# Performance work log

Measured on AMD Instinct MI355X. Metric: run time of the kernel, lower is better.

Reference implementation:

```python
import jax, jax.numpy as jnp
import numpy as np

K = 2  # top-k experts per token


def setup_inputs() -> dict:
    key = jax.random.key(0)
    ks = jax.random.split(key, 5)
    N, D, F, E = 8192, 1024, 1024, 8
    s = lambda d: 1.0 / np.sqrt(d)
    return {
        "x": jax.random.normal(ks[0], (N, D), jnp.float32),
        "Wr": jax.random.normal(ks[1], (D, E), jnp.float32) * s(D),
        "br": jax.random.normal(ks[2], (E,), jnp.float32) * 0.01,
        "We": jax.random.normal(ks[3], (E, D, F), jnp.float32) * s(D),
        "be": jax.random.normal(ks[4], (E, F), jnp.float32) * 0.01,
    }


def reference(x, Wr, br, We, be):
    # Router: logits [N, E] -> top-k -> softmax over the k selected logits
    logits = x @ Wr + br
    topv, idx = jax.lax.top_k(logits, K)            # [N, K]
    w = jax.nn.softmax(topv, axis=-1)               # [N, K]
    # All-expert dense compute (eval mode: dropout is identity)
    h = jnp.einsum("nd,edf->nef", x, We) + be       # [N, E, F]
    h = jax.nn.gelu(h, approximate=False)           # exact GELU (torch nn.GELU default)
    # Gather the k selected experts per token and combine
    sel = jnp.take_along_axis(h, idx[:, :, None], axis=1)  # [N, K, F]
    out = jnp.einsum("nk,nkf->nf", w, sel)          # [N, F]
    return out
```

## Files before the change

kernel.cpp:

```cpp
#include <hip/hip_runtime.h>
#include <hip/hip_bf16.h>
#include <math.h>
#include <stdint.h>

#define N_TOK 8192
#define DIM   1024
#define FDIM  1024
#define NEXP  8

typedef unsigned short u16;
typedef __bf16 bf16x8 __attribute__((ext_vector_type(8)));
typedef float  f32x4  __attribute__((ext_vector_type(4)));

__device__ __forceinline__ u16 f2bf(float f) {
  union { float f; uint32_t u; } v; v.f = f;
  return (u16)((v.u + 0x7fffu + ((v.u >> 16) & 1u)) >> 16);
}

__global__ __launch_bounds__(256) void k_prep(
    const float* __restrict__ x, const float* __restrict__ Wr,
    const float* __restrict__ br, const float* __restrict__ We,
    u16* __restrict__ xb, u16* __restrict__ WeT,
    int* __restrict__ topk_idx, float* __restrict__ topk_w0) {
  __shared__ float tile[64][65];
  int b = blockIdx.x;
  if (b < 2048) {
    int n = b * 4 + (threadIdx.x >> 6);
    int lane = threadIdx.x & 63;
    const float4* xr = (const float4*)(x + (size_t)n * DIM);
    ushort4* xbr = (ushort4*)(xb + (size_t)n * DIM);
    double acc[8];
#pragma unroll
    for (int e = 0; e < 8; ++e) acc[e] = 0.0;
#pragma unroll
    for (int i = 0; i < 4; ++i) {
      int d4 = lane + 64 * i;
      float4 v = xr[d4];
      ushort4 o;
      o.x = f2bf(v.x); o.y = f2bf(v.y); o.z = f2bf(v.z); o.w = f2bf(v.w);
      xbr[d4] = o;
      float vv[4] = {v.x, v.y, v.z, v.w};
      const float* wr = Wr + (size_t)d4 * 4 * NEXP;
#pragma unroll
      for (int j = 0; j < 4; ++j) {
        float4 w0 = *(const float4*)(wr + j * 8);
        float4 w1 = *(const float4*)(wr + j * 8 + 4);
        acc[0] += (double)vv[j] * w0.x; acc[1] += (double)vv[j] * w0.y;
        acc[2] += (double)vv[j] * w0.z; acc[3] += (double)vv[j] * w0.w;
        acc[4] += (double)vv[j] * w1.x; acc[5] += (double)vv[j] * w1.y;
        acc[6] += (double)vv[j] * w1.z; acc[7] += (double)vv[j] * w1.w;
      }
    }
#pragma unroll
    for (int e = 0; e < 8; ++e) {
      for (int off = 32; off; off >>= 1) acc[e] += __shfl_xor(acc[e], off);
    }
    if (lane == 0) {
      double lg[8];
#pragma unroll
      for (int e = 0; e < 8; ++e) lg[e] = acc[e] + (double)br[e];
      int i0 = 0; double v0 = lg[0];
#pragma unroll
      for (int e = 1; e < 8; ++e) if (lg[e] > v0) { v0 = lg[e]; i0 = e; }
      int i1 = -1; double v1 = -1e300;
#pragma unroll
      for (int e = 0; e < 8; ++e) if (e != i0 && lg[e] > v1) { v1 = lg[e]; i1 = e; }
      float w0 = 1.0f / (1.0f + expf((float)(v1 - v0)));
      topk_idx[n] = i0 | (i1 << 8);
      topk_w0[n] = w0;
    }
  } else {
    int tb = b - 2048;
    int e = tb >> 8;
    int d0 = ((tb >> 4) & 15) * 64, f0 = (tb & 15) * 64;
    int t = threadIdx.x;
    int lr = t >> 6, lc = t & 63;
    const float* src = We + (size_t)e * DIM * FDIM + (size_t)d0 * FDIM + f0;
#pragma unroll
    for (int i = 0; i < 16; ++i)
      tile[i * 4 + lr][lc] = src[(size_t)(i * 4 + lr) * FDIM + lc];
    __syncthreads();
    u16* dst = WeT + (size_t)e * FDIM * DIM + (size_t)f0 * DIM + d0;
#pragma unroll
    for (int i = 0; i < 16; ++i)
      dst[(size_t)(i * 4 + lr) * DIM + lc] = f2bf(tile[lc][i * 4 + lr]);
  }
}

__global__ __launch_bounds__(256) void k_build_lists(const int* __restrict__ topk_idx,
                                                     int* __restrict__ gcount,
                                                     int* __restrict__ token_list) {
  __shared__ int lcount[8];
  __shared__ int lbase[8];
  int t = threadIdx.x;
  int n = blockIdx.x * 256 + t;
  if (t < 8) lcount[t] = 0;
  __syncthreads();
  int pk = topk_idx[n];
  int e0 = pk & 0xff, e1 = (pk >> 8) & 0xff;
  int p0 = atomicAdd(&lcount[e0], 1);
  int p1 = atomicAdd(&lcount[e1], 1);
  __syncthreads();
  if (t < 8) lbase[t] = atomicAdd(&gcount[t], lcount[t]);
  __syncthreads();
  token_list[e0 * N_TOK + lbase[e0] + p0] = n * 2;
  token_list[e1 * N_TOK + lbase[e1] + p1] = n * 2 + 1;
}

#define BM 256
#define BN 128
#define BK 64
#define NWG 576
#define NTHR 512

__global__ __launch_bounds__(NTHR, 4) void k_moe_gemm(
    const u16* __restrict__ xb, const u16* __restrict__ WeT,
    const float* __restrict__ be, const int* __restrict__ gcount,
    const int* __restrict__ token_list, u16* __restrict__ hbuf) {
  int b = blockIdx.x;
  int w = (b & 7) * (NWG / 8) + (b >> 3);
  int e = -1, my = 0, fx = 0, cnt = 0, pfx = 0;
#pragma unroll
  for (int i = 0; i < NEXP; ++i) {
    int c = gcount[i];
    int tiles = ((c + BM - 1) >> 8) * (FDIM / BN);
    if (e < 0 && w < pfx + tiles) {
      e = i; int lw = w - pfx; my = lw >> 3; fx = lw & 7; cnt = c;
    }
    pfx += tiles;
  }
  if (e < 0) return;
  int m0 = my * BM, f0 = fx * BN;

  __shared__ u16 sA[BM * BK];
  __shared__ u16 sB[BN * BK];

  int tid = threadIdx.x;
  int lane = tid & 63, wid = tid >> 6;
  int wm = wid >> 1, wn = wid & 1;
  int rA = lane & 15, kg = lane >> 4;

  const int* tl = token_list + e * N_TOK;

  const u16* aA[4];
  const u16* aB[2];
  int cnt1 = cnt - 1;
#pragma unroll
  for (int it = 0; it < 4; ++it) {
    int c = it * NTHR + tid;
    int row = c >> 3, cj = c & 7;
    int sw = (cj * 8) ^ ((row & 7) << 3);
    int slot = m0 + row; if (slot > cnt1) slot = cnt1;
    int tok = tl[slot] >> 1;
    aA[it] = xb + (size_t)tok * DIM + sw;
  }
#pragma unroll
  for (int it = 0; it < 2; ++it) {
    int c = it * NTHR + tid;
    int row = c >> 3, cj = c & 7;
    int sw = (cj * 8) ^ ((row & 7) << 3);
    aB[it] = WeT + ((size_t)(e * FDIM + f0 + row)) * DIM + sw;
  }

  f32x4 zero = {0.f, 0.f, 0.f, 0.f};
  f32x4 acc[4][4];
#pragma unroll
  for (int mi = 0; mi < 4; ++mi)
#pragma unroll
    for (int ni = 0; ni < 4; ++ni) acc[mi][ni] = zero;

  const char* pA = (const char*)sA + (wm * 64 + rA) * 128;
  const char* pB = (const char*)sB + (wn * 64 + rA) * 128;
  int swz = (rA & 7) << 4;

  for (int kt = 0; kt < DIM / BK; ++kt) {
    int k0 = kt * BK;
#pragma unroll
    for (int it = 0; it < 4; ++it)
      __builtin_amdgcn_global_load_lds(
          (const __attribute__((address_space(1))) void*)(aA[it] + k0),
          (__attribute__((address_space(3))) void*)(sA + (it * NTHR + tid) * 8), 16, 0, 0);
#pragma unroll
    for (int it = 0; it < 2; ++it)
      __builtin_amdgcn_global_load_lds(
          (const __attribute__((address_space(1))) void*)(aB[it] + k0),
          (__attribute__((address_space(3))) void*)(sB + (it * NTHR + tid) * 8), 16, 0, 0);
    __syncthreads();
#pragma unroll
    for (int kk = 0; kk < 2; ++kk) {
      int kb = ((kk << 6) | (kg << 4)) ^ swz;
      bf16x8 av[4], bv[4];
#pragma unroll
      for (int mi = 0; mi < 4; ++mi)
        av[mi] = *(const bf16x8*)(pA + mi * 2048 + kb);
#pragma unroll
      for (int ni = 0; ni < 4; ++ni)
        bv[ni] = *(const bf16x8*)(pB + ni * 2048 + kb);
#pragma unroll
      for (int mi = 0; mi < 4; ++mi)
#pragma unroll
        for (int ni = 0; ni < 4; ++ni)
          acc[mi][ni] = __builtin_amdgcn_mfma_f32_16x16x32_bf16(av[mi], bv[ni], acc[mi][ni], 0, 0, 0);
    }
    __syncthreads();
  }

  const float* bptr = be + e * FDIM;
  int colf = f0 + wn * 64 + rA;
#pragma unroll
  for (int mi = 0; mi < 4; ++mi) {
#pragma unroll
    for (int j = 0; j < 4; ++j) {
      int slot = m0 + wm * 64 + mi * 16 + kg * 4 + j;
      if (slot < cnt) {
        int tok2 = tl[slot];
        u16* hrow = hbuf + (size_t)tok2 * FDIM;
#pragma unroll
        for (int ni = 0; ni < 4; ++ni) {
          int f = colf + ni * 16;
          float v = acc[mi][ni][j] + bptr[f];
          float g = 0.5f * v * (1.0f + erff(v * 0.70710678118654752f));
          hrow[f] = f2bf(g);
        }
      }
    }
  }
}

__global__ __launch_bounds__(256) void k_combine(const u16* __restrict__ hbuf,
                                                 const float* __restrict__ topk_w0,
                                                 float* __restrict__ out) {
  int n = blockIdx.x * 2 + (threadIdx.x >> 7);
  int t = threadIdx.x & 127;
  float w0 = topk_w0[n], w1 = 1.0f - w0;
  const bf16x8* r0 = (const bf16x8*)(hbuf + (size_t)(2 * n) * FDIM);
  const bf16x8* r1 = (const bf16x8*)(hbuf + (size_t)(2 * n + 1) * FDIM);
  bf16x8 a = r0[t], c = r1[t];
  float o[8];
#pragma unroll
  for (int i = 0; i < 8; ++i) o[i] = w0 * (float)a[i] + w1 * (float)c[i];
  float* orow = out + (size_t)n * FDIM + t * 8;
  *(float4*)(orow)     = *(float4*)(o);
  *(float4*)(orow + 4) = *(float4*)(o + 4);
}

extern "C" void kernel_launch(void* const* d_in, const int* in_sizes, int n_in,
                              void* d_out, int out_size, void* d_ws, size_t ws_size,
                              hipStream_t stream) {
  const float* x  = (const float*)d_in[0];
  const float* Wr = (const float*)d_in[1];
  const float* br = (const float*)d_in[2];
  const float* We = (const float*)d_in[3];
  const float* be = (const float*)d_in[4];
  float* out = (float*)d_out;

  char* ws = (char*)d_ws;
  u16* xb = (u16*)ws;                ws += (size_t)N_TOK * DIM * 2;
  u16* WeT = (u16*)ws;               ws += (size_t)NEXP * FDIM * DIM * 2;
  u16* hbuf = (u16*)ws;              ws += (size_t)2 * N_TOK * FDIM * 2;
  int* token_list = (int*)ws;        ws += (size_t)NEXP * N_TOK * 4;
  int* topk_idx = (int*)ws;          ws += (size_t)N_TOK * 4;
  float* topk_w0 = (float*)ws;       ws += (size_t)N_TOK * 4;
  int* gcount = (int*)ws;

  hipMemsetAsync(gcount, 0, NEXP * sizeof(int), stream);

  k_prep<<<dim3(4096), dim3(256), 0, stream>>>(x, Wr, br, We, xb, WeT, topk_idx, topk_w0);
  k_build_lists<<<dim3(N_TOK / 256), dim3(256), 0, stream>>>(topk_idx, gcount, token_list);
  k_moe_gemm<<<dim3(NWG), dim3(NTHR), 0, stream>>>(xb, WeT, be, gcount, token_list, hbuf);
  k_combine<<<dim3(N_TOK / 2), dim3(256), 0, stream>>>(hbuf, topk_w0, out);
}
```

Measured before the change: 137.2 us.

## Double-buffer LDS in MoE GEMM and retile to 192x128 with 256 threads

Reworks the grouped expert GEMM to use two LDS buffers. The global-to-LDS load of the next K slice is issued before computing the current one, which removes one barrier per iteration and overlaps load latency with MFMA work. The tile changes from 256x128 with 512 threads to 192x128 with 256 threads: each wave now holds a 96x64 accumulator, and the grid grows to 744 workgroups for finer M granularity with less padding waste. The cost is doubled LDS use and more accumulator registers per thread, which may lower occupancy.

```diff
diff --git a/kernel.cpp b/kernel.cpp
--- a/kernel.cpp
+++ b/kernel.cpp
@@ -107,13 +107,12 @@
   token_list[e1 * N_TOK + lbase[e1] + p1] = n * 2 + 1;
 }
 
-#define BM 256
+#define BM 192
 #define BN 128
 #define BK 64
-#define NWG 576
-#define NTHR 512
-
-__global__ __launch_bounds__(NTHR, 4) void k_moe_gemm(
+#define NWG 744
+
+__global__ __launch_bounds__(256, 2) void k_moe_gemm(
     const u16* __restrict__ xb, const u16* __restrict__ WeT,
     const float* __restrict__ be, const int* __restrict__ gcount,
     const int* __restrict__ token_list, u16* __restrict__ hbuf) {
@@ -123,7 +122,7 @@
 #pragma unroll
   for (int i = 0; i < NEXP; ++i) {
     int c = gcount[i];
-    int tiles = ((c + BM - 1) >> 8) * (FDIM / BN);
+    int tiles = ((c + BM - 1) / BM) * (FDIM / BN);
     if (e < 0 && w < pfx + tiles) {
       e = i; int lw = w - pfx; my = lw >> 3; fx = lw & 7; cnt = c;
     }
@@ -132,8 +131,8 @@
   if (e < 0) return;
   int m0 = my * BM, f0 = fx * BN;
 
-  __shared__ u16 sA[BM * BK];
-  __shared__ u16 sB[BN * BK];
+  __shared__ u16 sA[2 * BM * BK];
+  __shared__ u16 sB[2 * BN * BK];
 
   int tid = threadIdx.x;
   int lane = tid & 63, wid = tid >> 6;
@@ -142,12 +141,12 @@
 
   const int* tl = token_list + e * N_TOK;
 
-  const u16* aA[4];
-  const u16* aB[2];
+  const u16* aA[6];
+  const u16* aB[4];
   int cnt1 = cnt - 1;
 #pragma unroll
-  for (int it = 0; it < 4; ++it) {
-    int c = it * NTHR + tid;
+  for (int it = 0; it < 6; ++it) {
+    int c = it * 256 + tid;
     int row = c >> 3, cj = c & 7;
     int sw = (cj * 8) ^ ((row & 7) << 3);
     int slot = m0 + row; if (slot > cnt1) slot = cnt1;
@@ -155,63 +154,74 @@
     aA[it] = xb + (size_t)tok * DIM + sw;
   }
 #pragma unroll
-  for (int it = 0; it < 2; ++it) {
-    int c = it * NTHR + tid;
+  for (int it = 0; it < 4; ++it) {
+    int c = it * 256 + tid;
     int row = c >> 3, cj = c & 7;
     int sw = (cj * 8) ^ ((row & 7) << 3);
     aB[it] = WeT + ((size_t)(e * FDIM + f0 + row)) * DIM + sw;
   }
 
-  f32x4 zero = {0.f, 0.f, 0.f, 0.f};
-  f32x4 acc[4][4];
-#pragma unroll
-  for (int mi = 0; mi < 4; ++mi)
-#pragma unroll
-    for (int ni = 0; ni < 4; ++ni) acc[mi][ni] = zero;
-
-  const char* pA = (const char*)sA + (wm * 64 + rA) * 128;
-  const char* pB = (const char*)sB + (wn * 64 + rA) * 128;
-  int swz = (rA & 7) << 4;
-
-  for (int kt = 0; kt < DIM / BK; ++kt) {
-    int k0 = kt * BK;
+  auto stage = [&](int buf, int k0) {
+#pragma unroll
+    for (int it = 0; it < 6; ++it)
+      __builtin_amdgcn_global_load_lds(
+          (const __attribute__((address_space(1))) void*)(aA[it] + k0),
+          (__attribute__((address_space(3))) void*)(sA + buf * (BM * BK) + (it * 256 + tid) * 8),
+          16, 0, 0);
 #pragma unroll
     for (int it = 0; it < 4; ++it)
       __builtin_amdgcn_global_load_lds(
-          (const __attribute__((address_space(1))) void*)(aA[it] + k0),
-          (__attribute__((address_space(3))) void*)(sA + (it * NTHR + tid) * 8), 16, 0, 0);
-#pragma unroll
-    for (int it = 0; it < 2; ++it)
-      __builtin_amdgcn_global_load_lds(
           (const __attribute__((address_space(1))) void*)(aB[it] + k0),
-          (__attribute__((address_space(3))) void*)(sB + (it * NTHR + tid) * 8), 16, 0, 0);
-    __syncthreads();
+          (__attribute__((address_space(3))) void*)(sB + buf * (BN * BK) + (it * 256 + tid) * 8),
+          16, 0, 0);
+  };
+
+  f32x4 zero = {0.f, 0.f, 0.f, 0.f};
+  f32x4 acc[6][4];
+#pragma unroll
+  for (int mi = 0; mi < 6; ++mi)
+#pragma unroll
+    for (int ni = 0; ni < 4; ++ni) acc[mi][ni] = zero;
+
+  int swz = (rA & 7) << 4;
+  int offA = (wm * 96 + rA) * 128;
+  int offB = (wn * 64 + rA) * 128;
+
+  stage(0, 0);
+  __syncthreads();
+
+  int buf = 0;
+  for (int kt = 0; kt < DIM / BK; ++kt) {
+    if (kt + 1 < DIM / BK) stage(buf ^ 1, (kt + 1) * BK);
+    const char* pA = (const char*)sA + buf * (BM * BK * 2) + offA;
+    const char* pB = (const char*)sB + buf * (BN * BK * 2) + offB;
 #pragma unroll
     for (int kk = 0; kk < 2; ++kk) {
       int kb = ((kk << 6) | (kg << 4)) ^ swz;
-      bf16x8 av[4], bv[4];
-#pragma unroll
-      for (int mi = 0; mi < 4; ++mi)
+      bf16x8 av[6], bv[4];
+#pragma unroll
+      for (int mi = 0; mi < 6; ++mi)
         av[mi] = *(const bf16x8*)(pA + mi * 2048 + kb);
 #pragma unroll
       for (int ni = 0; ni < 4; ++ni)
         bv[ni] = *(const bf16x8*)(pB + ni * 2048 + kb);
 #pragma unroll
-      for (int mi = 0; mi < 4; ++mi)
+      for (int mi = 0; mi < 6; ++mi)
 #pragma unroll
         for (int ni = 0; ni < 4; ++ni)
           acc[mi][ni] = __builtin_amdgcn_mfma_f32_16x16x32_bf16(av[mi], bv[ni], acc[mi][ni], 0, 0, 0);
     }
     __syncthreads();
+    buf ^= 1;
   }
 
   const float* bptr = be + e * FDIM;
   int colf = f0 + wn * 64 + rA;
 #pragma unroll
-  for (int mi = 0; mi < 4; ++mi) {
+  for (int mi = 0; mi < 6; ++mi) {
 #pragma unroll
     for (int j = 0; j < 4; ++j) {
-      int slot = m0 + wm * 64 + mi * 16 + kg * 4 + j;
+      int slot = m0 + wm * 96 + mi * 16 + kg * 4 + j;
       if (slot < cnt) {
         int tok2 = tl[slot];
         u16* hrow = hbuf + (size_t)tok2 * FDIM;
@@ -267,6 +277,6 @@
 
   k_prep<<<dim3(4096), dim3(256), 0, stream>>>(x, Wr, br, We, xb, WeT, topk_idx, topk_w0);
   k_build_lists<<<dim3(N_TOK / 256), dim3(256), 0, stream>>>(topk_idx, gcount, token_list);
-  k_moe_gemm<<<dim3(NWG), dim3(NTHR), 0, stream>>>(xb, WeT, be, gcount, token_list, hbuf);
+  k_moe_gemm<<<dim3(NWG), dim3(256), 0, stream>>>(xb, WeT, be, gcount, token_list, hbuf);
   k_combine<<<dim3(N_TOK / 2), dim3(256), 0, stream>>>(hbuf, topk_w0, out);
 }
```

New measurement: 151.0 us. 10.1% more time.
